# Performance work log

Hardware: AMD Instinct MI355X
Metric: run time of the kernel (lower is better)

## Reference

```python
import jax, jax.numpy as jnp
import numpy as np

D_MODEL = 256
NHEAD = 8
HEAD_DIM = D_MODEL // NHEAD
CLIP = 10.0


def setup_inputs() -> dict:
    key = jax.random.key(0)
    k1, k2, k3, k4 = jax.random.split(key, 4)
    B, N = 4, 256
    nodes = jax.random.normal(k1, (B, N, D_MODEL), dtype=jnp.float32)
    edges = jax.random.normal(k2, (B, N, N, D_MODEL), dtype=jnp.float32)
    # torch nn.Linear default init: U(-1/sqrt(in), 1/sqrt(in))
    bound = 1.0 / np.sqrt(D_MODEL)
    W = jax.random.uniform(k3, (D_MODEL, D_MODEL), minval=-bound, maxval=bound, dtype=jnp.float32)
    b = jax.random.uniform(k4, (D_MODEL,), minval=-bound, maxval=bound, dtype=jnp.float32)
    return {"nodes": nodes, "edges": edges, "W": W, "b": b}


def reference(nodes, edges, W, b):
    B, N, _ = nodes.shape
    H, Dh = NHEAD, HEAD_DIM

    def proj(x):  # torch Linear: x @ W.T + b
        return x @ W.T + b

    # Node projections: the module applies the SAME linear to q, k, v
    node_p = proj(nodes).reshape(B, N, H, Dh)
    nq, nk, nv = node_p, node_p, node_p
    # Edge projections (same linear for q and k)
    edge_p = proj(edges).reshape(B, N, N, H, Dh)
    eq, ek = edge_p, edge_p

    query = eq + nq[:, :, None, :, :]   # (B,N,N,H,Dh)
    key = ek + nk[:, None, :, :, :]     # (B,N,N,H,Dh)
    scores = jnp.einsum('bijhd,bijhd->bhij', query, key) / np.sqrt(Dh).astype(np.float32)
    scores = CLIP * jnp.tanh(scores)
    attn = jax.nn.softmax(scores, axis=-1)  # (B,H,N,N)
    # output = attn @ values (values transposed to (B,H,N,Dh))
    out = jnp.einsum('bhij,bjhd->bihd', attn, nv).reshape(B, N, D_MODEL)
    out = proj(out)
    return (out, attn)
```

## Files before the change

### kernel.cpp

```cpp
#include <hip/hip_runtime.h>
#include <hip/hip_bf16.h>
#include <math.h>

typedef short short8 __attribute__((ext_vector_type(8)));
typedef float f32x4 __attribute__((ext_vector_type(4)));

__device__ __forceinline__ unsigned short f2bf(float x) {
    unsigned u = __float_as_uint(x);
    u += 0x7FFF + ((u >> 16) & 1);
    return (unsigned short)(u >> 16);
}
__device__ __forceinline__ float bf2f(unsigned short h) {
    return __uint_as_float(((unsigned)h) << 16);
}

__device__ __forceinline__ void cvtpair(float f0, float f1, unsigned& hw, unsigned& lw) {
    __hip_bfloat162 h2 = __float22bfloat162_rn(float2{f0, f1});
    unsigned hu = *(unsigned*)&h2;
    float r0 = f0 - __uint_as_float(hu << 16);
    float r1 = f1 - __uint_as_float(hu & 0xFFFF0000u);
    __hip_bfloat162 l2 = __float22bfloat162_rn(float2{r0, r1});
    hw = hu;
    lw = *(unsigned*)&l2;
}

__device__ __forceinline__ void cvt8(const float4 a, const float4 b, short8& hi, short8& lo) {
    union { unsigned u[4]; short8 s; } H, L;
    cvtpair(a.x, a.y, H.u[0], L.u[0]);
    cvtpair(a.z, a.w, H.u[1], L.u[1]);
    cvtpair(b.x, b.y, H.u[2], L.u[2]);
    cvtpair(b.z, b.w, H.u[3], L.u[3]);
    hi = H.s; lo = L.s;
}

__device__ __forceinline__ float tanh10(float y) {
    float e = __expf(2.f * y);
    return 10.f * (e - 1.f) / (e + 1.f);
}

__global__ __launch_bounds__(256) void k_prep(const float* __restrict__ W,
                                              float* __restrict__ Wt,
                                              unsigned short* __restrict__ Whi,
                                              unsigned short* __restrict__ Wlo) {
    int d = blockIdx.x, k = threadIdx.x;
    float w = W[d * 256 + k];
    Wt[k * 256 + d] = w;
    unsigned short hi = f2bf(w);
    Whi[d * 256 + k] = hi;
    Wlo[d * 256 + k] = f2bf(w - bf2f(hi));
}

__global__ __launch_bounds__(256) void k_node_proj(const float* __restrict__ nodes,
                                                   const float* __restrict__ Wt,
                                                   const float* __restrict__ bias,
                                                   float* __restrict__ np_) {
    int row = blockIdx.x;
    int d = threadIdx.x;
    __shared__ float xl[256];
    xl[d] = nodes[row * 256 + d];
    __syncthreads();
    float a[8] = {0.f, 0.f, 0.f, 0.f, 0.f, 0.f, 0.f, 0.f};
#pragma unroll 4
    for (int k = 0; k < 256; k += 8) {
#pragma unroll
        for (int q = 0; q < 8; ++q)
            a[q] = fmaf(xl[k + q], Wt[(k + q) * 256 + d], a[q]);
    }
    np_[row * 256 + d] =
        bias[d] + ((a[0] + a[1]) + (a[2] + a[3])) + ((a[4] + a[5]) + (a[6] + a[7]));
}

__global__ __launch_bounds__(256, 2) void k_edge_mfma(const float* __restrict__ edges,
                                                      const unsigned short* __restrict__ Whi,
                                                      const unsigned short* __restrict__ Wlo,
                                                      const float* __restrict__ bias,
                                                      const float* __restrict__ np_,
                                                      float* __restrict__ attn) {
    __shared__ float npi[128];
    __shared__ float sc[4][256];

    const int t = threadIdx.x;
    const int w = t >> 6, l = t & 63;
    const int col = l & 15, g = l >> 4;

    const int p = blockIdx.x;
    const int L = (p & 7) * 256 + (p >> 3);
    const int tile = L >> 1, half = L & 1;
    const int bb = tile >> 8, ii = tile & 255;
    const int n0 = half * 128;

    if (t < 32)
        ((float4*)npi)[t] = ((const float4*)(np_ + (size_t)(bb * 256 + ii) * 256 + n0))[t];

    f32x4 acc[4][8];
#pragma unroll
    for (int mt = 0; mt < 4; ++mt)
#pragma unroll
        for (int nt = 0; nt < 8; ++nt) acc[mt][nt] = (f32x4){0.f, 0.f, 0.f, 0.f};

    const float* ea = edges + ((size_t)((bb * 256 + ii) * 256 + w * 64 + col)) * 256 + g * 8;
    const int lidx = col * 256 + g * 8;

    float4 e[4][2];
#pragma unroll
    for (int mt = 0; mt < 4; ++mt) {
        e[mt][0] = *(const float4*)(ea + mt * 4096);
        e[mt][1] = *(const float4*)(ea + mt * 4096 + 4);
    }
    short8 Bh = *(const short8*)(Whi + (size_t)(n0 * 256) + lidx);
    short8 Bl = *(const short8*)(Wlo + (size_t)(n0 * 256) + lidx);

    short8 Ah[4], Al[4];

    for (int kc = 0; kc < 8; ++kc) {
#pragma unroll
        for (int mt = 0; mt < 4; ++mt)
            cvt8(e[mt][0], e[mt][1], Ah[mt], Al[mt]);
        if (kc < 7) {
#pragma unroll
            for (int mt = 0; mt < 4; ++mt) {
                e[mt][0] = *(const float4*)(ea + (kc + 1) * 32 + mt * 4096);
                e[mt][1] = *(const float4*)(ea + (kc + 1) * 32 + mt * 4096 + 4);
            }
        }
#pragma unroll
        for (int nt = 0; nt < 8; ++nt) {
            short8 cBh = Bh, cBl = Bl;
            const int nt2 = (nt + 1) & 7;
            const int kc2 = (nt == 7) ? kc + 1 : kc;
            const size_t wofs = (size_t)((n0 + nt2 * 16) * 256 + kc2 * 32);
            Bh = *(const short8*)(Whi + wofs + lidx);
            Bl = *(const short8*)(Wlo + wofs + lidx);
#pragma unroll
            for (int mt = 0; mt < 4; ++mt) {
                acc[mt][nt] = __builtin_amdgcn_mfma_f32_16x16x32_bf16(Ah[mt], cBh, acc[mt][nt], 0, 0, 0);
                acc[mt][nt] = __builtin_amdgcn_mfma_f32_16x16x32_bf16(Ah[mt], cBl, acc[mt][nt], 0, 0, 0);
                acc[mt][nt] = __builtin_amdgcn_mfma_f32_16x16x32_bf16(Al[mt], cBh, acc[mt][nt], 0, 0, 0);
            }
        }
    }

    __syncthreads();

    const float isq = 0.17677669529663687f;
    float bv[8], nv[8];
#pragma unroll
    for (int nt = 0; nt < 8; ++nt) {
        int dl = nt * 16 + col;
        bv[nt] = bias[n0 + dl];
        nv[nt] = npi[dl];
    }
#pragma unroll
    for (int mt = 0; mt < 4; ++mt) {
#pragma unroll
        for (int r = 0; r < 4; ++r) {
            int el = w * 64 + mt * 16 + g * 4 + r;
            const float* npj = np_ + (size_t)(bb * 256 + el) * 256 + n0;
            float pp, s0 = 0.f, s1 = 0.f, s2 = 0.f, s3 = 0.f;
            pp = acc[mt][0][r] + bv[0]; s0 += (pp + nv[0]) * (pp + npj[col]);
            pp = acc[mt][1][r] + bv[1]; s0 += (pp + nv[1]) * (pp + npj[16 + col]);
            pp = acc[mt][2][r] + bv[2]; s1 += (pp + nv[2]) * (pp + npj[32 + col]);
            pp = acc[mt][3][r] + bv[3]; s1 += (pp + nv[3]) * (pp + npj[48 + col]);
            pp = acc[mt][4][r] + bv[4]; s2 += (pp + nv[4]) * (pp + npj[64 + col]);
            pp = acc[mt][5][r] + bv[5]; s2 += (pp + nv[5]) * (pp + npj[80 + col]);
            pp = acc[mt][6][r] + bv[6]; s3 += (pp + nv[6]) * (pp + npj[96 + col]);
            pp = acc[mt][7][r] + bv[7]; s3 += (pp + nv[7]) * (pp + npj[112 + col]);
#pragma unroll
            for (int m = 1; m < 16; m <<= 1) {
                s0 += __shfl_xor(s0, m, 64);
                s1 += __shfl_xor(s1, m, 64);
                s2 += __shfl_xor(s2, m, 64);
                s3 += __shfl_xor(s3, m, 64);
            }
            if (col == 0) {
                sc[0][el] = tanh10(s0 * isq);
                sc[1][el] = tanh10(s1 * isq);
                sc[2][el] = tanh10(s2 * isq);
                sc[3][el] = tanh10(s3 * isq);
            }
        }
    }
    __syncthreads();

    {
        float4 v = *(float4*)&sc[w][l * 4];
        float m = fmaxf(fmaxf(v.x, v.y), fmaxf(v.z, v.w));
#pragma unroll
        for (int s = 1; s < 64; s <<= 1) m = fmaxf(m, __shfl_xor(m, s, 64));
        v.x = __expf(v.x - m); v.y = __expf(v.y - m);
        v.z = __expf(v.z - m); v.w = __expf(v.w - m);
        float sum = v.x + v.y + v.z + v.w;
#pragma unroll
        for (int s = 1; s < 64; s <<= 1) sum += __shfl_xor(sum, s, 64);
        float inv = 1.f / sum;
        v.x *= inv; v.y *= inv; v.z *= inv; v.w *= inv;
        *(float4*)(attn + (((size_t)(bb * 8 + half * 4 + w) * 256 + ii) << 8) + l * 4) = v;
    }
}

__global__ __launch_bounds__(256) void k_out(const float* __restrict__ attn,
                                             const float* __restrict__ np_,
                                             const float* __restrict__ Wt,
                                             const float* __restrict__ bias,
                                             float* __restrict__ out) {
    int bi = blockIdx.x;
    int bb = bi >> 8, ii = bi & 255;
    int d = threadIdx.x;
    __shared__ float at[8 * 256];
    __shared__ float xl[256];
#pragma unroll
    for (int s = 0; s < 2; ++s) {
        int idx = d + s * 256;
        int h = idx >> 6, q = idx & 63;
        ((float4*)at)[idx] =
            ((const float4*)(attn + ((size_t)(bb * 8 + h) * 256 + ii) * 256))[q];
    }
    __syncthreads();
    int h = d >> 5;
    const float* npb = np_ + (size_t)bb * 65536 + d;
    const float* ath = at + h * 256;
    float a[8] = {0.f, 0.f, 0.f, 0.f, 0.f, 0.f, 0.f, 0.f};
#pragma unroll 2
    for (int j = 0; j < 256; j += 8) {
#pragma unroll
        for (int q = 0; q < 8; ++q)
            a[q] = fmaf(ath[j + q], npb[(size_t)(j + q) * 256], a[q]);
    }
    xl[d] = ((a[0] + a[1]) + (a[2] + a[3])) + ((a[4] + a[5]) + (a[6] + a[7]));
    __syncthreads();
    float c[8] = {bias[d], 0.f, 0.f, 0.f, 0.f, 0.f, 0.f, 0.f};
#pragma unroll 2
    for (int k = 0; k < 256; k += 8) {
#pragma unroll
        for (int q = 0; q < 8; ++q)
            c[q] = fmaf(xl[k + q], Wt[(k + q) * 256 + d], c[q]);
    }
    out[bi * 256 + d] =
        ((c[0] + c[1]) + (c[2] + c[3])) + ((c[4] + c[5]) + (c[6] + c[7]));
}

extern "C" void kernel_launch(void* const* d_in, const int* in_sizes, int n_in,
                              void* d_out, int out_size, void* d_ws, size_t ws_size,
                              hipStream_t stream) {
    (void)in_sizes; (void)n_in; (void)out_size; (void)ws_size;
    const float* nodes = (const float*)d_in[0];
    const float* edges = (const float*)d_in[1];
    const float* W     = (const float*)d_in[2];
    const float* bias  = (const float*)d_in[3];

    float* out  = (float*)d_out;
    float* attn = out + 262144;

    float* np_ = (float*)d_ws;
    float* Wt  = np_ + 262144;
    unsigned short* Whi = (unsigned short*)(Wt + 65536);
    unsigned short* Wlo = Whi + 65536;

    hipLaunchKernelGGL(k_prep,      dim3(256),  dim3(256), 0, stream, W, Wt, Whi, Wlo);
    hipLaunchKernelGGL(k_node_proj, dim3(1024), dim3(256), 0, stream, nodes, Wt, bias, np_);
    hipLaunchKernelGGL(k_edge_mfma, dim3(2048), dim3(256), 0, stream, edges, Whi, Wlo, bias, np_, attn);
    hipLaunchKernelGGL(k_out,       dim3(1024), dim3(256), 0, stream, attn, np_, Wt, bias, out);
}
```

Measured before the change: 543.0 us.

## Stage W tiles in LDS via async global_load_lds double buffering

The hi/lo bf16 weight tiles were previously loaded per-thread from global memory with a software prefetch. Now each k-chunk of W is copied straight into a double-buffered LDS tile with global_load_lds and read back from LDS for the MFMAs. The weight layout is XOR-swizzled in the prep kernel to avoid LDS bank conflicts, and s_setprio is raised around the MFMA loop. The aim is to cut redundant global/L2 traffic for W across waves and overlap the weight loads with compute. In exchange it adds about 32KB of LDS per block, which may reduce occupancy, and depends on hand-written vmcnt waits and barriers being correct.

```diff
diff --git a/kernel.cpp b/kernel.cpp
--- a/kernel.cpp
+++ b/kernel.cpp
@@ -38,6 +38,11 @@
     return 10.f * (e - 1.f) / (e + 1.f);
 }
 
+#define GLDS16(gp, lp)                                                        \
+    __builtin_amdgcn_global_load_lds(                                         \
+        (const __attribute__((address_space(1))) void*)(gp),                  \
+        (__attribute__((address_space(3))) void*)(lp), 16, 0, 0)
+
 __global__ __launch_bounds__(256) void k_prep(const float* __restrict__ W,
                                               float* __restrict__ Wt,
                                               unsigned short* __restrict__ Whi,
@@ -46,8 +51,11 @@
     float w = W[d * 256 + k];
     Wt[k * 256 + d] = w;
     unsigned short hi = f2bf(w);
-    Whi[d * 256 + k] = hi;
-    Wlo[d * 256 + k] = f2bf(w - bf2f(hi));
+    int s  = (k >> 3) & 3;
+    int sp = s ^ ((d >> 1) & 3);
+    int idx = d * 256 + (k & ~31) + sp * 8 + (k & 7);
+    Whi[idx] = hi;
+    Wlo[idx] = f2bf(w - bf2f(hi));
 }
 
 __global__ __launch_bounds__(256) void k_node_proj(const float* __restrict__ nodes,
@@ -76,12 +84,14 @@
                                                       const float* __restrict__ bias,
                                                       const float* __restrict__ np_,
                                                       float* __restrict__ attn) {
+    __shared__ unsigned short Wbuf[2][2][128 * 32];
     __shared__ float npi[128];
     __shared__ float sc[4][256];
 
     const int t = threadIdx.x;
     const int w = t >> 6, l = t & 63;
     const int col = l & 15, g = l >> 4;
+    const int wrow = l >> 2, wq = l & 3;
 
     const int p = blockIdx.x;
     const int L = (p & 7) * 256 + (p >> 3);
@@ -91,6 +101,7 @@
 
     if (t < 32)
         ((float4*)npi)[t] = ((const float4*)(np_ + (size_t)(bb * 256 + ii) * 256 + n0))[t];
+    __builtin_amdgcn_sched_barrier(0);
 
     f32x4 acc[4][8];
 #pragma unroll
@@ -99,48 +110,68 @@
         for (int nt = 0; nt < 8; ++nt) acc[mt][nt] = (f32x4){0.f, 0.f, 0.f, 0.f};
 
     const float* ea = edges + ((size_t)((bb * 256 + ii) * 256 + w * 64 + col)) * 256 + g * 8;
-    const int lidx = col * 256 + g * 8;
-
+    const size_t wg0 = (size_t)(n0 + w * 32 + wrow) * 256 + wq * 8;
+    const size_t wg1 = wg0 + 16 * 256;
+
+    GLDS16(Whi + wg0, &Wbuf[0][0][(w * 32) * 32]);
+    GLDS16(Wlo + wg0, &Wbuf[0][1][(w * 32) * 32]);
+    GLDS16(Whi + wg1, &Wbuf[0][0][(w * 32 + 16) * 32]);
+    GLDS16(Wlo + wg1, &Wbuf[0][1][(w * 32 + 16) * 32]);
+    __builtin_amdgcn_sched_barrier(0);
     float4 e[4][2];
 #pragma unroll
     for (int mt = 0; mt < 4; ++mt) {
         e[mt][0] = *(const float4*)(ea + mt * 4096);
         e[mt][1] = *(const float4*)(ea + mt * 4096 + 4);
     }
-    short8 Bh = *(const short8*)(Whi + (size_t)(n0 * 256) + lidx);
-    short8 Bl = *(const short8*)(Wlo + (size_t)(n0 * 256) + lidx);
+    __builtin_amdgcn_sched_barrier(0);
+    asm volatile("s_waitcnt vmcnt(8)\n\ts_barrier" ::: "memory");
+
+    const int swb = (g ^ ((col >> 1) & 3)) << 3;
 
     short8 Ah[4], Al[4];
 
+#pragma unroll
     for (int kc = 0; kc < 8; ++kc) {
 #pragma unroll
         for (int mt = 0; mt < 4; ++mt)
             cvt8(e[mt][0], e[mt][1], Ah[mt], Al[mt]);
+        __builtin_amdgcn_sched_barrier(0);
         if (kc < 7) {
+            const int nb = (kc + 1) & 1;
+            const size_t kofs = (size_t)(kc + 1) * 32;
+            GLDS16(Whi + wg0 + kofs, &Wbuf[nb][0][(w * 32) * 32]);
+            GLDS16(Wlo + wg0 + kofs, &Wbuf[nb][1][(w * 32) * 32]);
+            GLDS16(Whi + wg1 + kofs, &Wbuf[nb][0][(w * 32 + 16) * 32]);
+            GLDS16(Wlo + wg1 + kofs, &Wbuf[nb][1][(w * 32 + 16) * 32]);
+            __builtin_amdgcn_sched_barrier(0);
 #pragma unroll
             for (int mt = 0; mt < 4; ++mt) {
                 e[mt][0] = *(const float4*)(ea + (kc + 1) * 32 + mt * 4096);
                 e[mt][1] = *(const float4*)(ea + (kc + 1) * 32 + mt * 4096 + 4);
             }
-        }
+            __builtin_amdgcn_sched_barrier(0);
+        }
+        const unsigned short* bh = &Wbuf[kc & 1][0][0] + col * 32 + swb;
+        const unsigned short* bl = &Wbuf[kc & 1][1][0] + col * 32 + swb;
+        __builtin_amdgcn_s_setprio(1);
 #pragma unroll
         for (int nt = 0; nt < 8; ++nt) {
-            short8 cBh = Bh, cBl = Bl;
-            const int nt2 = (nt + 1) & 7;
-            const int kc2 = (nt == 7) ? kc + 1 : kc;
-            const size_t wofs = (size_t)((n0 + nt2 * 16) * 256 + kc2 * 32);
-            Bh = *(const short8*)(Whi + wofs + lidx);
-            Bl = *(const short8*)(Wlo + wofs + lidx);
+            short8 Bh = *(const short8*)(bh + nt * 512);
+            short8 Bl = *(const short8*)(bl + nt * 512);
 #pragma unroll
             for (int mt = 0; mt < 4; ++mt) {
-                acc[mt][nt] = __builtin_amdgcn_mfma_f32_16x16x32_bf16(Ah[mt], cBh, acc[mt][nt], 0, 0, 0);
-                acc[mt][nt] = __builtin_amdgcn_mfma_f32_16x16x32_bf16(Ah[mt], cBl, acc[mt][nt], 0, 0, 0);
-                acc[mt][nt] = __builtin_amdgcn_mfma_f32_16x16x32_bf16(Al[mt], cBh, acc[mt][nt], 0, 0, 0);
-            }
-        }
-    }
-
-    __syncthreads();
+                acc[mt][nt] = __builtin_amdgcn_mfma_f32_16x16x32_bf16(Ah[mt], Bh, acc[mt][nt], 0, 0, 0);
+                acc[mt][nt] = __builtin_amdgcn_mfma_f32_16x16x32_bf16(Ah[mt], Bl, acc[mt][nt], 0, 0, 0);
+                acc[mt][nt] = __builtin_amdgcn_mfma_f32_16x16x32_bf16(Al[mt], Bh, acc[mt][nt], 0, 0, 0);
+            }
+        }
+        __builtin_amdgcn_s_setprio(0);
+        __builtin_amdgcn_sched_barrier(0);
+        if (kc < 7) {
+            asm volatile("s_waitcnt vmcnt(8)\n\ts_barrier" ::: "memory");
+        }
+    }
 
     const float isq = 0.17677669529663687f;
     float bv[8], nv[8];
```

Result: faster. 478.1 us (-12.0%).
